# Kernel tuning notes

Hardware: AMD Instinct MI355X
Metric: run time of the kernel (lower is better)

## Reference

```python
import jax, jax.numpy as jnp
import numpy as np

EMBED_DIM = 1024
NUM_HEADS = 16
HEAD_DIM = EMBED_DIM // NUM_HEADS
B, SQ, SKV = 2, 2048, 2048


def setup_inputs() -> dict:
    key = jax.random.key(0)
    ks = jax.random.split(key, 12)
    s = 1.0 / np.sqrt(EMBED_DIM)
    inp = {
        "query": jax.random.normal(ks[0], (B, SQ, EMBED_DIM), jnp.float32),
        "key": jax.random.normal(ks[1], (B, SKV, EMBED_DIM), jnp.float32),
        "value": jax.random.normal(ks[2], (B, SKV, EMBED_DIM), jnp.float32),
        "Wq": jax.random.normal(ks[3], (EMBED_DIM, EMBED_DIM), jnp.float32) * s,
        "bq": jnp.zeros((EMBED_DIM,), jnp.float32),
        "Wk": jax.random.normal(ks[4], (EMBED_DIM, EMBED_DIM), jnp.float32) * s,
        "bk": jnp.zeros((EMBED_DIM,), jnp.float32),
        "Wv": jax.random.normal(ks[5], (EMBED_DIM, EMBED_DIM), jnp.float32) * s,
        "bv": jnp.zeros((EMBED_DIM,), jnp.float32),
        "Wo": jax.random.normal(ks[6], (EMBED_DIM, EMBED_DIM), jnp.float32) * s,
        "bo": jnp.zeros((EMBED_DIM,), jnp.float32),
        "ln_gamma": jnp.ones((EMBED_DIM,), jnp.float32),
        "ln_beta": jnp.zeros((EMBED_DIM,), jnp.float32),
    }
    return inp


def reference(query, key, value, Wq, bq, Wk, bk, Wv, bv, Wo, bo, ln_gamma, ln_beta):
    b, sq, d = query.shape
    skv = key.shape[1]
    residual = query
    # projections -> [b, h, s, hd]
    Q = (query @ Wq + bq).reshape(b, sq, NUM_HEADS, HEAD_DIM).transpose(0, 2, 1, 3)
    K = (key @ Wk + bk).reshape(b, skv, NUM_HEADS, HEAD_DIM).transpose(0, 2, 1, 3)
    V = (value @ Wv + bv).reshape(b, skv, NUM_HEADS, HEAD_DIM).transpose(0, 2, 1, 3)
    scores = jnp.einsum("bhqd,bhkd->bhqk", Q, K) / jnp.sqrt(jnp.float32(HEAD_DIM)).astype(Q.dtype)
    attn = jax.nn.softmax(scores, axis=-1)  # dropout identity in eval
    attended = jnp.einsum("bhqk,bhkd->bhqd", attn, V)
    attended = attended.transpose(0, 2, 1, 3).reshape(b, sq, d)
    out = attended @ Wo + bo
    x = out + residual
    mu = jnp.mean(x, axis=-1, keepdims=True)
    var = jnp.var(x, axis=-1, keepdims=True)
    return (x - mu) / jnp.sqrt(var + 1e-5) * ln_gamma + ln_beta
```

## Files before the change

kernel.cpp:

```cpp
#include <hip/hip_runtime.h>

#define EMBED 1024
#define NHEAD 16
#define HDIM  64
#define BATCH 2
#define SEQ   2048
#define ROWS  (BATCH*SEQ)

typedef __bf16 bf16x8 __attribute__((ext_vector_type(8)));
typedef float  f32x4  __attribute__((ext_vector_type(4)));
typedef float  f32x16 __attribute__((ext_vector_type(16)));
typedef unsigned short u16x8 __attribute__((ext_vector_type(8)));
typedef unsigned short u16x4 __attribute__((ext_vector_type(4)));
typedef unsigned int   u32x2 __attribute__((ext_vector_type(2)));

__device__ __forceinline__ unsigned short f2bf(float f) {
    unsigned int u = __float_as_uint(f);
    u += 0x7FFFu + ((u >> 16) & 1u);
    return (unsigned short)(u >> 16);
}
__device__ __forceinline__ unsigned int pk2(float a, float b) {
    return (__float_as_uint(b) & 0xFFFF0000u) | (__float_as_uint(a) >> 16);
}
__device__ __forceinline__ f32x4 zero4() { f32x4 z = {0.f, 0.f, 0.f, 0.f}; return z; }

__device__ __forceinline__ void gl_lds16(const unsigned short* g, unsigned short* l) {
    __builtin_amdgcn_global_load_lds(
        (const __attribute__((address_space(1))) void*)g,
        (__attribute__((address_space(3))) void*)l, 16, 0, 0);
}

__global__ __launch_bounds__(256) void cvt3_kernel(const float* __restrict__ q,
                                                   const float* __restrict__ k,
                                                   const float* __restrict__ v,
                                                   unsigned short* __restrict__ qo,
                                                   unsigned short* __restrict__ ko,
                                                   unsigned short* __restrict__ vo) {
    const float* in; unsigned short* out;
    if (blockIdx.y == 0)      { in = q; out = qo; }
    else if (blockIdx.y == 1) { in = k; out = ko; }
    else                      { in = v; out = vo; }
    int i = (blockIdx.x * 256 + threadIdx.x) * 4;
    float4 vv = *(const float4*)(in + i);
    u16x4 o = {f2bf(vv.x), f2bf(vv.y), f2bf(vv.z), f2bf(vv.w)};
    *(u16x4*)(out + i) = o;
}

__global__ __launch_bounds__(256) void transpose4_kernel(const float* __restrict__ w0,
                                                         const float* __restrict__ w1,
                                                         const float* __restrict__ w2,
                                                         const float* __restrict__ w3,
                                                         unsigned short* __restrict__ o0,
                                                         unsigned short* __restrict__ o1,
                                                         unsigned short* __restrict__ o2,
                                                         unsigned short* __restrict__ o3) {
    const float* in; unsigned short* out;
    if (blockIdx.z == 0)      { in = w0; out = o0; }
    else if (blockIdx.z == 1) { in = w1; out = o1; }
    else if (blockIdx.z == 2) { in = w2; out = o2; }
    else                      { in = w3; out = o3; }
    __shared__ float tile[32][33];
    int tx = threadIdx.x, ty = threadIdx.y;
    int x = blockIdx.x * 32 + tx;
    int y0 = blockIdx.y * 32 + ty;
#pragma unroll
    for (int r = 0; r < 4; ++r)
        tile[ty + 8 * r][tx] = in[(size_t)(y0 + 8 * r) * EMBED + x];
    __syncthreads();
    int ox = blockIdx.y * 32 + tx;
    int oy = blockIdx.x * 32 + ty;
#pragma unroll
    for (int r = 0; r < 4; ++r)
        out[(size_t)(oy + 8 * r) * EMBED + ox] = f2bf(tile[tx][ty + 8 * r]);
}

__global__ __launch_bounds__(256, 3) void gemm_qkv_kernel(
    const unsigned short* __restrict__ qb, const unsigned short* __restrict__ kb,
    const unsigned short* __restrict__ vb,
    const unsigned short* __restrict__ Wqt, const unsigned short* __restrict__ Wkt,
    const unsigned short* __restrict__ Wvt,
    const float* __restrict__ bq, const float* __restrict__ bk, const float* __restrict__ bv,
    unsigned short* __restrict__ Qp, unsigned short* __restrict__ Kp,
    unsigned short* __restrict__ Vtb) {
    __shared__ unsigned short As[2][4096];
    __shared__ unsigned short Bs[2][4096];
    const unsigned short *A, *Bt; const float* bias; void* outp; int mode; float osc;
    if (blockIdx.z == 0)      { A = qb; Bt = Wqt; bias = bq; outp = Qp;  mode = 0; osc = 0.125f; }
    else if (blockIdx.z == 1) { A = kb; Bt = Wkt; bias = bk; outp = Kp;  mode = 0; osc = 1.0f; }
    else                      { A = vb; Bt = Wvt; bias = bv; outp = Vtb; mode = 1; osc = 1.0f; }

    const int t = threadIdx.x;
    const int m0 = blockIdx.y * 128, n0 = blockIdx.x * 128;
    const int wave = t >> 6, lane = t & 63;
    const int wr = wave >> 1, wc = wave & 1;
    const int lm = lane & 15, lq = lane >> 4;
    const int sr = t >> 2;
    const int csrc = (t & 3) ^ ((sr >> 1) & 3);
    const int pa = lq ^ ((lm >> 1) & 3);

    const unsigned short* gA = A + (size_t)(m0 + sr) * EMBED + csrc * 8;
    const unsigned short* gB = Bt + (size_t)(n0 + sr) * EMBED + csrc * 8;

    f32x4 acc[4][4];
#pragma unroll
    for (int i = 0; i < 4; ++i)
#pragma unroll
        for (int j = 0; j < 4; ++j) acc[i][j] = zero4();

    gl_lds16(gA,             As[0] + wave * 512);
    gl_lds16(gA + 64 * EMBED, As[0] + 2048 + wave * 512);
    gl_lds16(gB,             Bs[0] + wave * 512);
    gl_lds16(gB + 64 * EMBED, Bs[0] + 2048 + wave * 512);

    for (int kk = 0; kk < 32; ++kk) {
        __syncthreads();
        if (kk < 31) {
            gA += 32; gB += 32;
            const int nb = (kk + 1) & 1;
            gl_lds16(gA,             As[nb] + wave * 512);
            gl_lds16(gA + 64 * EMBED, As[nb] + 2048 + wave * 512);
            gl_lds16(gB,             Bs[nb] + wave * 512);
            gl_lds16(gB + 64 * EMBED, Bs[nb] + 2048 + wave * 512);
        }
        const unsigned short* Ac = As[kk & 1];
        const unsigned short* Bc = Bs[kk & 1];
        bf16x8 af[4], bfr[4];
#pragma unroll
        for (int i = 0; i < 4; ++i)
            af[i] = *(const bf16x8*)&Ac[(wr * 64 + i * 16 + lm) * 32 + pa * 8];
#pragma unroll
        for (int j = 0; j < 4; ++j)
            bfr[j] = *(const bf16x8*)&Bc[(wc * 64 + j * 16 + lm) * 32 + pa * 8];
#pragma unroll
        for (int i = 0; i < 4; ++i)
#pragma unroll
            for (int j = 0; j < 4; ++j)
                acc[i][j] = __builtin_amdgcn_mfma_f32_16x16x32_bf16(af[i], bfr[j], acc[i][j], 0, 0, 0);
    }

#pragma unroll
    for (int i = 0; i < 4; ++i)
#pragma unroll
        for (int j = 0; j < 4; ++j) {
            int n = n0 + wc * 64 + j * 16 + lm;
            float bn = bias[n];
#pragma unroll
            for (int r = 0; r < 4; ++r) {
                int m = m0 + wr * 64 + i * 16 + lq * 4 + r;
                float v = acc[i][j][r] + bn;
                int b = m >> 11, s = m & 2047, h = n >> 6, hd = n & 63;
                if (mode == 0)
                    ((unsigned short*)outp)[((size_t)((b * NHEAD + h) * SEQ + s) << 6) + hd] = f2bf(v * osc);
                else
                    ((unsigned short*)outp)[(size_t)((b * NHEAD + h) * HDIM + hd) * SEQ + s] = f2bf(v);
            }
        }
}

__global__ __launch_bounds__(256, 2) void gemm_o_kernel(
    const unsigned short* __restrict__ att, const unsigned short* __restrict__ Wot,
    const float* __restrict__ bo, float* __restrict__ xbuf,
    const float* __restrict__ residual) {
    __shared__ unsigned short As[2][2048];
    __shared__ unsigned short Bs[2][4096];
    const int t = threadIdx.x;
    const int m0 = blockIdx.y * 64, n0 = blockIdx.x * 128;
    const int wave = t >> 6, lane = t & 63;
    const int lm = lane & 15, lq = lane >> 4;
    const int sr = t >> 2;
    const int csrc = (t & 3) ^ ((sr >> 1) & 3);
    const int pa = lq ^ ((lm >> 1) & 3);

    const unsigned short* gA = att + (size_t)(m0 + sr) * EMBED + csrc * 8;
    const unsigned short* gB = Wot + (size_t)(n0 + sr) * EMBED + csrc * 8;

    f32x4 acc[4][2];
#pragma unroll
    for (int i = 0; i < 4; ++i)
#pragma unroll
        for (int j = 0; j < 2; ++j) acc[i][j] = zero4();

    gl_lds16(gA,             As[0] + wave * 512);
    gl_lds16(gB,             Bs[0] + wave * 512);
    gl_lds16(gB + 64 * EMBED, Bs[0] + 2048 + wave * 512);

    for (int kk = 0; kk < 32; ++kk) {
        __syncthreads();
        if (kk < 31) {
            gA += 32; gB += 32;
            const int nb = (kk + 1) & 1;
            gl_lds16(gA,             As[nb] + wave * 512);
            gl_lds16(gB,             Bs[nb] + wave * 512);
            gl_lds16(gB + 64 * EMBED, Bs[nb] + 2048 + wave * 512);
        }
        const unsigned short* Ac = As[kk & 1];
        const unsigned short* Bc = Bs[kk & 1];
        bf16x8 af[4], bfr[2];
#pragma unroll
        for (int i = 0; i < 4; ++i)
            af[i] = *(const bf16x8*)&Ac[(i * 16 + lm) * 32 + pa * 8];
#pragma unroll
        for (int j = 0; j < 2; ++j)
            bfr[j] = *(const bf16x8*)&Bc[(wave * 32 + j * 16 + lm) * 32 + pa * 8];
#pragma unroll
        for (int i = 0; i < 4; ++i)
#pragma unroll
            for (int j = 0; j < 2; ++j)
                acc[i][j] = __builtin_amdgcn_mfma_f32_16x16x32_bf16(af[i], bfr[j], acc[i][j], 0, 0, 0);
    }

#pragma unroll
    for (int i = 0; i < 4; ++i)
#pragma unroll
        for (int j = 0; j < 2; ++j) {
            int n = n0 + wave * 32 + j * 16 + lm;
            float bn = bo[n];
#pragma unroll
            for (int r = 0; r < 4; ++r) {
                int m = m0 + i * 16 + lq * 4 + r;
                size_t idx = (size_t)m * EMBED + n;
                xbuf[idx] = acc[i][j][r] + bn + residual[idx];
            }
        }
}

__global__ __launch_bounds__(256, 2) void attn_kernel(const unsigned short* __restrict__ Qp,
                                                      const unsigned short* __restrict__ Kp,
                                                      const unsigned short* __restrict__ Vt,
                                                      unsigned short* __restrict__ att) {
    __shared__ unsigned short Ks[2][4096];
    __shared__ unsigned short Vs[2][4096];
    __shared__ unsigned short Ps[8192];
    const int t = threadIdx.x;
    const int bh = blockIdx.x;
    const int b = bh >> 4, h = bh & 15;
    const int q0 = blockIdx.y * 128;
    const unsigned short* Qh = Qp + (size_t)bh * SEQ * HDIM;
    const unsigned short* Kh = Kp + (size_t)bh * SEQ * HDIM;
    const unsigned short* Vh = Vt + (size_t)bh * HDIM * SEQ;
    const int wave = t >> 6, lane = t & 63;
    const int ln31 = lane & 31, half = lane >> 5;

    bf16x8 qf[4];
    {
        const unsigned short* qptr = Qh + (size_t)(q0 + wave * 32 + ln31) * HDIM + half * 8;
#pragma unroll
        for (int s = 0; s < 4; ++s) qf[s] = *(const bf16x8*)(qptr + s * 16);
    }

    const int q8a = t, q8b = 256 + t;
    const int fa = q8a >> 6, fb = q8b >> 6;
    const int ma = q8a & 31, mb = q8b & 31;
    const int ha = (q8a >> 5) & 1, hb = (q8b >> 5) & 1;
    const unsigned short* gK0 = Kh + (size_t)((fa >> 2) * 32 + ma) * HDIM + (fa & 3) * 16 + ha * 8;
    const unsigned short* gK1 = Kh + (size_t)((fb >> 2) * 32 + mb) * HDIM + (fb & 3) * 16 + hb * 8;
    const unsigned short* gV0 = Vh + (size_t)((fa >> 2) * 32 + ma) * SEQ + (fa & 3) * 16 + ha * 8;
    const unsigned short* gV1 = Vh + (size_t)((fb >> 2) * 32 + mb) * SEQ + (fb & 3) * 16 + hb * 8;

    gl_lds16(gK0, Ks[0] + wave * 512);
    gl_lds16(gK1, Ks[0] + 2048 + wave * 512);
    gl_lds16(gV0, Vs[0] + wave * 512);
    gl_lds16(gV1, Vs[0] + 2048 + wave * 512);

    f32x16 Oacc[2];
#pragma unroll
    for (int mt = 0; mt < 2; ++mt)
#pragma unroll
        for (int r = 0; r < 16; ++r) Oacc[mt][r] = 0.f;
    float l_run = 0.f;

    unsigned short* PsW = Ps + wave * 2048;

    for (int kt = 0; kt < 32; ++kt) {
        __syncthreads();
        if (kt < 31) {
            gK0 += 64 * HDIM; gK1 += 64 * HDIM; gV0 += 64; gV1 += 64;
            const int nb = (kt + 1) & 1;
            gl_lds16(gK0, Ks[nb] + wave * 512);
            gl_lds16(gK1, Ks[nb] + 2048 + wave * 512);
            gl_lds16(gV0, Vs[nb] + wave * 512);
            gl_lds16(gV1, Vs[nb] + 2048 + wave * 512);
        }
        const unsigned short* Kc = Ks[kt & 1];
        const unsigned short* Vc = Vs[kt & 1];

        f32x16 S[2];
#pragma unroll
        for (int mt = 0; mt < 2; ++mt) {
#pragma unroll
            for (int r = 0; r < 16; ++r) S[mt][r] = 0.f;
#pragma unroll
            for (int s = 0; s < 4; ++s) {
                bf16x8 af = *(const bf16x8*)&Kc[(mt * 4 + s) * 512 + half * 256 + ln31 * 8];
                S[mt] = __builtin_amdgcn_mfma_f32_32x32x16_bf16(af, qf[s], S[mt], 0, 0, 0);
            }
        }

        float rs = 0.f;
#pragma unroll
        for (int mt = 0; mt < 2; ++mt)
#pragma unroll
            for (int r = 0; r < 16; ++r) {
                float p = __expf(S[mt][r] - 12.f);
                S[mt][r] = p;
                rs += p;
            }
        rs += __shfl_xor(rs, 32);
        l_run += rs;

#pragma unroll
        for (int mt = 0; mt < 2; ++mt)
#pragma unroll
            for (int rg = 0; rg < 4; ++rg) {
                u32x2 pw = {pk2(S[mt][rg * 4 + 0], S[mt][rg * 4 + 1]),
                            pk2(S[mt][rg * 4 + 2], S[mt][rg * 4 + 3])};
                *(u32x2*)&PsW[(2 * mt + (rg >> 1)) * 512 + (rg & 1) * 256 + ln31 * 8 + half * 4] = pw;
            }

#pragma unroll
        for (int sp = 0; sp < 4; ++sp) {
            bf16x8 bp = *(const bf16x8*)&PsW[sp * 512 + half * 256 + ln31 * 8];
#pragma unroll
            for (int mt = 0; mt < 2; ++mt) {
                bf16x8 av = *(const bf16x8*)&Vc[(mt * 4 + sp) * 512 + half * 256 + ln31 * 8];
                Oacc[mt] = __builtin_amdgcn_mfma_f32_32x32x16_bf16(av, bp, Oacc[mt], 0, 0, 0);
            }
        }
    }

    float inv = 1.f / l_run;
    int q = q0 + wave * 32 + ln31;
    unsigned short* orow = att + (size_t)(b * SEQ + q) * EMBED + h * HDIM;
#pragma unroll
    for (int mt = 0; mt < 2; ++mt)
#pragma unroll
        for (int rg = 0; rg < 4; ++rg) {
            u16x4 ow = {f2bf(Oacc[mt][rg * 4 + 0] * inv), f2bf(Oacc[mt][rg * 4 + 1] * inv),
                        f2bf(Oacc[mt][rg * 4 + 2] * inv), f2bf(Oacc[mt][rg * 4 + 3] * inv)};
            *(u16x4*)&orow[mt * 32 + rg * 8 + half * 4] = ow;
        }
}

__global__ __launch_bounds__(256) void ln_kernel(const float* __restrict__ x,
                                                 const float* __restrict__ gamma,
                                                 const float* __restrict__ beta,
                                                 float* __restrict__ out) {
    __shared__ float red[8];
    const int row = blockIdx.x, t = threadIdx.x;
    float4 v = *(const float4*)(x + (size_t)row * EMBED + t * 4);
    float s = v.x + v.y + v.z + v.w;
    float ss = v.x * v.x + v.y * v.y + v.z * v.z + v.w * v.w;
#pragma unroll
    for (int o = 1; o < 64; o <<= 1) {
        s += __shfl_xor(s, o);
        ss += __shfl_xor(ss, o);
    }
    int wave = t >> 6, lane = t & 63;
    if (lane == 0) { red[wave] = s; red[4 + wave] = ss; }
    __syncthreads();
    s = red[0] + red[1] + red[2] + red[3];
    ss = red[4] + red[5] + red[6] + red[7];
    float mu = s * (1.f / EMBED);
    float var = ss * (1.f / EMBED) - mu * mu;
    float rstd = rsqrtf(var + 1e-5f);
    float4 g = *(const float4*)(gamma + t * 4);
    float4 bb = *(const float4*)(beta + t * 4);
    float4 o;
    o.x = (v.x - mu) * rstd * g.x + bb.x;
    o.y = (v.y - mu) * rstd * g.y + bb.y;
    o.z = (v.z - mu) * rstd * g.z + bb.z;
    o.w = (v.w - mu) * rstd * g.w + bb.w;
    *(float4*)(out + (size_t)row * EMBED + t * 4) = o;
}

extern "C" void kernel_launch(void* const* d_in, const int* in_sizes, int n_in,
                              void* d_out, int out_size, void* d_ws, size_t ws_size,
                              hipStream_t stream) {
    const float* query = (const float*)d_in[0];
    const float* key_  = (const float*)d_in[1];
    const float* value = (const float*)d_in[2];
    const float* Wq = (const float*)d_in[3];
    const float* bq = (const float*)d_in[4];
    const float* Wk = (const float*)d_in[5];
    const float* bk = (const float*)d_in[6];
    const float* Wv = (const float*)d_in[7];
    const float* bv = (const float*)d_in[8];
    const float* Wo = (const float*)d_in[9];
    const float* bo = (const float*)d_in[10];
    const float* gamma = (const float*)d_in[11];
    const float* beta  = (const float*)d_in[12];

    char* ws = (char*)d_ws;
    const size_t MB = 1024 * 1024;
    unsigned short* qb  = (unsigned short*)(ws + 0);
    unsigned short* kb  = (unsigned short*)(ws + 8 * MB);
    unsigned short* vb  = (unsigned short*)(ws + 16 * MB);
    unsigned short* Wqt = (unsigned short*)(ws + 24 * MB);
    unsigned short* Wkt = (unsigned short*)(ws + 26 * MB);
    unsigned short* Wvt = (unsigned short*)(ws + 28 * MB);
    unsigned short* Wot = (unsigned short*)(ws + 30 * MB);
    unsigned short* Qp  = (unsigned short*)(ws + 32 * MB);
    unsigned short* Kp  = (unsigned short*)(ws + 40 * MB);
    unsigned short* Vtb = (unsigned short*)(ws + 48 * MB);
    unsigned short* att = (unsigned short*)(ws + 0);
    float*          xbuf = (float*)(ws + 8 * MB);

    cvt3_kernel<<<dim3(4096, 3), 256, 0, stream>>>(query, key_, value, qb, kb, vb);
    transpose4_kernel<<<dim3(32, 32, 4), dim3(32, 8), 0, stream>>>(Wq, Wk, Wv, Wo, Wqt, Wkt, Wvt, Wot);

    gemm_qkv_kernel<<<dim3(8, 32, 3), 256, 0, stream>>>(qb, kb, vb, Wqt, Wkt, Wvt,
                                                        bq, bk, bv, Qp, Kp, Vtb);

    attn_kernel<<<dim3(32, 16), 256, 0, stream>>>(Qp, Kp, Vtb, att);

    gemm_o_kernel<<<dim3(8, 64), 256, 0, stream>>>(att, Wot, bo, xbuf, query);
    ln_kernel<<<ROWS, 256, 0, stream>>>(xbuf, gamma, beta, (float*)d_out);
}
```

Baseline: 257.0 us.

## Stage QKV GEMM epilogue through LDS for coalesced stores; swap grid order

The QKV projection epilogue now writes the bias-added bf16 results into shared memory in two half passes, then emits 16-byte vectorized stores. This gives contiguous rows for Q/K and contiguous sequence runs for the transposed V output, replacing scattered 2-byte stores. Both GEMMs swap grid axes so consecutive blocks walk M rather than N, which changes L2 reuse of the weight tiles. The QKV launch-bounds occupancy hint drops from 3 to 2 blocks, and the epilogue adds extra barriers.

```diff
diff --git a/kernel.cpp b/kernel.cpp
--- a/kernel.cpp
+++ b/kernel.cpp
@@ -74,7 +74,7 @@
         out[(size_t)(oy + 8 * r) * EMBED + ox] = f2bf(tile[tx][ty + 8 * r]);
 }
 
-__global__ __launch_bounds__(256, 3) void gemm_qkv_kernel(
+__global__ __launch_bounds__(256, 2) void gemm_qkv_kernel(
     const unsigned short* __restrict__ qb, const unsigned short* __restrict__ kb,
     const unsigned short* __restrict__ vb,
     const unsigned short* __restrict__ Wqt, const unsigned short* __restrict__ Wkt,
@@ -82,15 +82,14 @@
     const float* __restrict__ bq, const float* __restrict__ bk, const float* __restrict__ bv,
     unsigned short* __restrict__ Qp, unsigned short* __restrict__ Kp,
     unsigned short* __restrict__ Vtb) {
-    __shared__ unsigned short As[2][4096];
-    __shared__ unsigned short Bs[2][4096];
-    const unsigned short *A, *Bt; const float* bias; void* outp; int mode; float osc;
+    __shared__ unsigned short smem[16384];
+    const unsigned short *A, *Bt; const float* bias; unsigned short* outp; int mode; float osc;
     if (blockIdx.z == 0)      { A = qb; Bt = Wqt; bias = bq; outp = Qp;  mode = 0; osc = 0.125f; }
     else if (blockIdx.z == 1) { A = kb; Bt = Wkt; bias = bk; outp = Kp;  mode = 0; osc = 1.0f; }
     else                      { A = vb; Bt = Wvt; bias = bv; outp = Vtb; mode = 1; osc = 1.0f; }
 
     const int t = threadIdx.x;
-    const int m0 = blockIdx.y * 128, n0 = blockIdx.x * 128;
+    const int m0 = blockIdx.x * 128, n0 = blockIdx.y * 128;
     const int wave = t >> 6, lane = t & 63;
     const int wr = wave >> 1, wc = wave & 1;
     const int lm = lane & 15, lq = lane >> 4;
@@ -107,30 +106,29 @@
 #pragma unroll
         for (int j = 0; j < 4; ++j) acc[i][j] = zero4();
 
-    gl_lds16(gA,             As[0] + wave * 512);
-    gl_lds16(gA + 64 * EMBED, As[0] + 2048 + wave * 512);
-    gl_lds16(gB,             Bs[0] + wave * 512);
-    gl_lds16(gB + 64 * EMBED, Bs[0] + 2048 + wave * 512);
+    gl_lds16(gA,              smem + wave * 512);
+    gl_lds16(gA + 64 * EMBED, smem + 2048 + wave * 512);
+    gl_lds16(gB,              smem + 8192 + wave * 512);
+    gl_lds16(gB + 64 * EMBED, smem + 8192 + 2048 + wave * 512);
 
     for (int kk = 0; kk < 32; ++kk) {
         __syncthreads();
         if (kk < 31) {
             gA += 32; gB += 32;
-            const int nb = (kk + 1) & 1;
-            gl_lds16(gA,             As[nb] + wave * 512);
-            gl_lds16(gA + 64 * EMBED, As[nb] + 2048 + wave * 512);
-            gl_lds16(gB,             Bs[nb] + wave * 512);
-            gl_lds16(gB + 64 * EMBED, Bs[nb] + 2048 + wave * 512);
-        }
-        const unsigned short* Ac = As[kk & 1];
-        const unsigned short* Bc = Bs[kk & 1];
+            const int nbo = ((kk + 1) & 1) * 4096;
+            gl_lds16(gA,              smem + nbo + wave * 512);
+            gl_lds16(gA + 64 * EMBED, smem + nbo + 2048 + wave * 512);
+            gl_lds16(gB,              smem + 8192 + nbo + wave * 512);
+            gl_lds16(gB + 64 * EMBED, smem + 8192 + nbo + 2048 + wave * 512);
+        }
+        const int cbo = (kk & 1) * 4096;
         bf16x8 af[4], bfr[4];
 #pragma unroll
         for (int i = 0; i < 4; ++i)
-            af[i] = *(const bf16x8*)&Ac[(wr * 64 + i * 16 + lm) * 32 + pa * 8];
+            af[i] = *(const bf16x8*)&smem[cbo + (wr * 64 + i * 16 + lm) * 32 + pa * 8];
 #pragma unroll
         for (int j = 0; j < 4; ++j)
-            bfr[j] = *(const bf16x8*)&Bc[(wc * 64 + j * 16 + lm) * 32 + pa * 8];
+            bfr[j] = *(const bf16x8*)&smem[8192 + cbo + (wc * 64 + j * 16 + lm) * 32 + pa * 8];
 #pragma unroll
         for (int i = 0; i < 4; ++i)
 #pragma unroll
@@ -138,23 +136,64 @@
                 acc[i][j] = __builtin_amdgcn_mfma_f32_16x16x32_bf16(af[i], bfr[j], acc[i][j], 0, 0, 0);
     }
 
-#pragma unroll
-    for (int i = 0; i < 4; ++i)
-#pragma unroll
-        for (int j = 0; j < 4; ++j) {
-            int n = n0 + wc * 64 + j * 16 + lm;
-            float bn = bias[n];
-#pragma unroll
-            for (int r = 0; r < 4; ++r) {
-                int m = m0 + wr * 64 + i * 16 + lq * 4 + r;
-                float v = acc[i][j][r] + bn;
-                int b = m >> 11, s = m & 2047, h = n >> 6, hd = n & 63;
-                if (mode == 0)
-                    ((unsigned short*)outp)[((size_t)((b * NHEAD + h) * SEQ + s) << 6) + hd] = f2bf(v * osc);
-                else
-                    ((unsigned short*)outp)[(size_t)((b * NHEAD + h) * HDIM + hd) * SEQ + s] = f2bf(v);
-            }
-        }
+    const int row = t >> 2, seg = t & 3;
+    if (mode == 0) {
+#pragma unroll
+        for (int p = 0; p < 2; ++p) {
+            __syncthreads();
+            if (wr == p) {
+#pragma unroll
+                for (int i = 0; i < 4; ++i)
+#pragma unroll
+                    for (int j = 0; j < 4; ++j) {
+                        float bn = bias[n0 + wc * 64 + j * 16 + lm];
+                        int nl = wc * 64 + j * 16 + lm;
+#pragma unroll
+                        for (int r = 0; r < 4; ++r)
+                            smem[(i * 16 + lq * 4 + r) * 136 + nl] =
+                                f2bf((acc[i][j][r] + bn) * osc);
+                    }
+            }
+            __syncthreads();
+            int m = m0 + p * 64 + row;
+            int b = m >> 11, sI = m & 2047;
+            int ncol = n0 + seg * 32;
+            int h = ncol >> 6, hd0 = ncol & 63;
+            unsigned short* dst = outp + (((size_t)((b * NHEAD + h) * SEQ + sI)) << 6) + hd0;
+            const unsigned short* src = smem + row * 136 + seg * 32;
+            *(u16x8*)(dst)      = *(const u16x8*)(src);
+            *(u16x8*)(dst + 8)  = *(const u16x8*)(src + 8);
+            *(u16x8*)(dst + 16) = *(const u16x8*)(src + 16);
+            *(u16x8*)(dst + 24) = *(const u16x8*)(src + 24);
+        }
+    } else {
+#pragma unroll
+        for (int p = 0; p < 2; ++p) {
+            __syncthreads();
+            if (wc == p) {
+#pragma unroll
+                for (int i = 0; i < 4; ++i)
+#pragma unroll
+                    for (int j = 0; j < 4; ++j) {
+                        float bn = bias[n0 + p * 64 + j * 16 + lm];
+                        u16x4 pw = {f2bf(acc[i][j][0] + bn), f2bf(acc[i][j][1] + bn),
+                                    f2bf(acc[i][j][2] + bn), f2bf(acc[i][j][3] + bn)};
+                        *(u16x4*)&smem[(j * 16 + lm) * 136 + wr * 64 + i * 16 + lq * 4] = pw;
+                    }
+            }
+            __syncthreads();
+            int n = n0 + p * 64 + row;
+            int h = n >> 6, hd = n & 63;
+            int b = m0 >> 11;
+            int s0 = (m0 & 2047) + seg * 32;
+            unsigned short* dst = outp + ((size_t)((b * NHEAD + h) * HDIM + hd)) * SEQ + s0;
+            const unsigned short* src = smem + row * 136 + seg * 32;
+            *(u16x8*)(dst)      = *(const u16x8*)(src);
+            *(u16x8*)(dst + 8)  = *(const u16x8*)(src + 8);
+            *(u16x8*)(dst + 16) = *(const u16x8*)(src + 16);
+            *(u16x8*)(dst + 24) = *(const u16x8*)(src + 24);
+        }
+    }
 }
 
 __global__ __launch_bounds__(256, 2) void gemm_o_kernel(
@@ -164,7 +203,7 @@
     __shared__ unsigned short As[2][2048];
     __shared__ unsigned short Bs[2][4096];
     const int t = threadIdx.x;
-    const int m0 = blockIdx.y * 64, n0 = blockIdx.x * 128;
+    const int m0 = blockIdx.x * 64, n0 = blockIdx.y * 128;
     const int wave = t >> 6, lane = t & 63;
     const int lm = lane & 15, lq = lane >> 4;
     const int sr = t >> 2;
@@ -180,8 +219,8 @@
 #pragma unroll
         for (int j = 0; j < 2; ++j) acc[i][j] = zero4();
 
-    gl_lds16(gA,             As[0] + wave * 512);
-    gl_lds16(gB,             Bs[0] + wave * 512);
+    gl_lds16(gA,              As[0] + wave * 512);
+    gl_lds16(gB,              Bs[0] + wave * 512);
     gl_lds16(gB + 64 * EMBED, Bs[0] + 2048 + wave * 512);
 
     for (int kk = 0; kk < 32; ++kk) {
@@ -189,19 +228,18 @@
         if (kk < 31) {
             gA += 32; gB += 32;
             const int nb = (kk + 1) & 1;
-            gl_lds16(gA,             As[nb] + wave * 512);
-            gl_lds16(gB,             Bs[nb] + wave * 512);
+            gl_lds16(gA,              As[nb] + wave * 512);
+            gl_lds16(gB,              Bs[nb] + wave * 512);
             gl_lds16(gB + 64 * EMBED, Bs[nb] + 2048 + wave * 512);
         }
-        const unsigned short* Ac = As[kk & 1];
-        const unsigned short* Bc = Bs[kk & 1];
+        const int cb = kk & 1;
         bf16x8 af[4], bfr[2];
 #pragma unroll
         for (int i = 0; i < 4; ++i)
-            af[i] = *(const bf16x8*)&Ac[(i * 16 + lm) * 32 + pa * 8];
+            af[i] = *(const bf16x8*)&As[cb][(i * 16 + lm) * 32 + pa * 8];
 #pragma unroll
         for (int j = 0; j < 2; ++j)
-            bfr[j] = *(const bf16x8*)&Bc[(wave * 32 + j * 16 + lm) * 32 + pa * 8];
+            bfr[j] = *(const bf16x8*)&Bs[cb][(wave * 32 + j * 16 + lm) * 32 + pa * 8];
 #pragma unroll
         for (int i = 0; i < 4; ++i)
 #pragma unroll
@@ -281,8 +319,7 @@
             gl_lds16(gV0, Vs[nb] + wave * 512);
             gl_lds16(gV1, Vs[nb] + 2048 + wave * 512);
         }
-        const unsigned short* Kc = Ks[kt & 1];
-        const unsigned short* Vc = Vs[kt & 1];
+        const int cb = kt & 1;
 
         f32x16 S[2];
 #pragma unroll
@@ -291,7 +328,7 @@
             for (int r = 0; r < 16; ++r) S[mt][r] = 0.f;
 #pragma unroll
             for (int s = 0; s < 4; ++s) {
-                bf16x8 af = *(const bf16x8*)&Kc[(mt * 4 + s) * 512 + half * 256 + ln31 * 8];
+                bf16x8 af = *(const bf16x8*)&Ks[cb][(mt * 4 + s) * 512 + half * 256 + ln31 * 8];
                 S[mt] = __builtin_amdgcn_mfma_f32_32x32x16_bf16(af, qf[s], S[mt], 0, 0, 0);
             }
         }
@@ -322,7 +359,7 @@
             bf16x8 bp = *(const bf16x8*)&PsW[sp * 512 + half * 256 + ln31 * 8];
 #pragma unroll
             for (int mt = 0; mt < 2; ++mt) {
-                bf16x8 av = *(const bf16x8*)&Vc[(mt * 4 + sp) * 512 + half * 256 + ln31 * 8];
+                bf16x8 av = *(const bf16x8*)&Vs[cb][(mt * 4 + sp) * 512 + half * 256 + ln31 * 8];
                 Oacc[mt] = __builtin_amdgcn_mfma_f32_32x32x16_bf16(av, bp, Oacc[mt], 0, 0, 0);
             }
         }
@@ -408,11 +445,11 @@
     cvt3_kernel<<<dim3(4096, 3), 256, 0, stream>>>(query, key_, value, qb, kb, vb);
     transpose4_kernel<<<dim3(32, 32, 4), dim3(32, 8), 0, stream>>>(Wq, Wk, Wv, Wo, Wqt, Wkt, Wvt, Wot);
 
-    gemm_qkv_kernel<<<dim3(8, 32, 3), 256, 0, stream>>>(qb, kb, vb, Wqt, Wkt, Wvt,
+    gemm_qkv_kernel<<<dim3(32, 8, 3), 256, 0, stream>>>(qb, kb, vb, Wqt, Wkt, Wvt,
                                                         bq, bk, bv, Qp, Kp, Vtb);
 
     attn_kernel<<<dim3(32, 16), 256, 0, stream>>>(Qp, Kp, Vtb, att);
 
-    gemm_o_kernel<<<dim3(8, 64), 256, 0, stream>>>(att, Wot, bo, xbuf, query);
+    gemm_o_kernel<<<dim3(64, 8), 256, 0, stream>>>(att, Wot, bo, xbuf, query);
     ln_kernel<<<ROWS, 256, 0, stream>>>(xbuf, gamma, beta, (float*)d_out);
 }
```

Result: faster. 250.4 us (-2.6%).
